# Kernel tuning notes

Hardware: AMD Instinct MI355X
Metric: run time of the kernel (lower is better)

The kernel has to match this reference:

```python
import jax, jax.numpy as jnp
import numpy as np

NPOINT, NSAMPLE, RADIUS = 1024, 32, 0.2
BN_EPS = 1e-5


def _fps(xyz, npoint):
    # Farthest point sampling. Torch version starts from a random index; we use
    # index 0 deterministically (same algorithm, fixed seed point).
    B, N, _ = xyz.shape

    def step(carry, _):
        distance, farthest = carry                               # [B,N], [B]
        centroid = jnp.take_along_axis(xyz, farthest[:, None, None], axis=1)  # [B,1,3]
        d = jnp.sum((xyz - centroid) ** 2, axis=-1)              # [B,N]
        distance = jnp.minimum(distance, d)
        nxt = jnp.argmax(distance, axis=-1).astype(jnp.int32)
        return (distance, nxt), farthest

    init = (jnp.full((B, N), 1e10, xyz.dtype), jnp.zeros((B,), jnp.int32))
    _, cents = jax.lax.scan(step, init, None, length=npoint)     # [npoint,B]
    return jnp.transpose(cents)                                  # [B,npoint]


def _ball_query(radius, nsample, xyz, new_xyz):
    # Sort-based ball query, exactly as the torch reference (pad with first idx).
    B, N, _ = xyz.shape
    sq = -2.0 * jnp.einsum('bsc,bnc->bsn', new_xyz, xyz)
    sq = sq + jnp.sum(new_xyz ** 2, -1)[:, :, None] + jnp.sum(xyz ** 2, -1)[:, None, :]
    idx = jnp.where(sq > radius * radius, N, jnp.arange(N, dtype=jnp.int32))  # [B,S,N]
    idx = jnp.sort(idx, axis=-1)[:, :, :nsample]                 # [B,S,nsample]
    first = idx[:, :, :1]
    return jnp.where(idx == N, first, idx)


def setup_inputs() -> dict:
    key = jax.random.key(0)
    ks = jax.random.split(key, 4)
    B, N = 8, 8192
    d = {"x": jax.random.uniform(ks[0], (B, N, 3), jnp.float32)}
    mlp = [3, 64, 64, 128]
    for i in range(3):
        cin, cout = mlp[i], mlp[i + 1]
        d[f"W{i+1}"] = jax.random.normal(ks[i + 1], (cout, cin), jnp.float32) * 0.1
        d[f"b{i+1}"] = jnp.zeros((cout,), jnp.float32)
        d[f"g{i+1}"] = jnp.ones((cout,), jnp.float32)
        d[f"be{i+1}"] = jnp.zeros((cout,), jnp.float32)
    return d


def reference(x, W1, b1, g1, be1, W2, b2, g2, be2, W3, b3, g3, be3):
    # sample_and_group (points=None)
    cents = _fps(x, NPOINT)                                      # [B,npoint]
    new_x = jnp.take_along_axis(x, cents[:, :, None], axis=1)    # [B,npoint,3]
    idx = _ball_query(RADIUS, NSAMPLE, x, new_x)                 # [B,npoint,nsample]
    grouped = jax.vmap(lambda p, i: p[i])(x, idx)                # [B,npoint,nsample,3]
    h = jnp.transpose(grouped - new_x[:, :, None, :], (0, 3, 2, 1))  # [B,3,nsample,npoint]

    # grouped 1x1 conv + BatchNorm (training-mode batch stats) + ReLU
    for W, b, g, be in ((W1, b1, g1, be1), (W2, b2, g2, be2), (W3, b3, g3, be3)):
        y = jnp.einsum('bcns,oc->bons', h, W) + b[None, :, None, None]
        mean = jnp.mean(y, axis=(0, 2, 3), keepdims=True)
        var = jnp.mean((y - mean) ** 2, axis=(0, 2, 3), keepdims=True)
        h = jax.nn.relu(g[None, :, None, None] * (y - mean) * jax.lax.rsqrt(var + BN_EPS)
                        + be[None, :, None, None])

    out = jnp.transpose(jnp.max(h, axis=2), (0, 2, 1))           # [B,npoint,128]
    return new_x, out
```

## Files before the change

kernel.cpp:

```cpp
#include <hip/hip_runtime.h>
#include <stdint.h>

constexpr int NB = 8;
constexpr int NN = 8192;
constexpr int NS = 1024;
constexpr int NK = 32;
constexpr int PTOT = NB * NS * NK;

#define R2C 0.039999999105930328f

__device__ unsigned short g_cents[NB * NS];
__device__ unsigned short g_idx[NB * NS * NK];
__device__ float g_stat1[12];
__device__ float g_stat2[4160];
__device__ float g_stat3[4160];
__device__ float g_st1[128];
__device__ float g_st2[128];
__device__ float g_st3[256];

__global__ __launch_bounds__(256, 4) void k_zero(){
  const int tid = threadIdx.x;
  for (int i = tid; i < 4160; i += 256){ g_stat2[i] = 0.f; g_stat3[i] = 0.f; }
  if (tid < 12) g_stat1[tid] = 0.f;
}

template<int C, int R>
__device__ __forceinline__ void rstep64(uint32_t& kh, uint32_t& kl){
  uint32_t oh = (uint32_t)__builtin_amdgcn_update_dpp(0, (int)kh, C, R, 0xf, false);
  uint32_t ol = (uint32_t)__builtin_amdgcn_update_dpp(0, (int)kl, C, R, 0xf, false);
  uint64_t o = ((uint64_t)oh << 32) | ol;
  uint64_t k = ((uint64_t)kh << 32) | kl;
  if (o > k){ kh = oh; kl = ol; }
}

__global__ __launch_bounds__(512)
__attribute__((amdgpu_waves_per_eu(2, 2)))
void k_fps(const float* __restrict__ x){
  __shared__ float lp[NN * 3];
  __shared__ uint2 part[16];
  const int b = blockIdx.x;
  const int t = threadIdx.x;
  const int lane = t & 63;
  const int w = t >> 6;
  const float* xb = x + b * NN * 3;
  float px[16], py[16], pz[16], dd[16];
#pragma unroll
  for (int j = 0; j < 16; j++){
    int p = t + 512 * j;
    px[j] = xb[p*3+0]; py[j] = xb[p*3+1]; pz[j] = xb[p*3+2];
    dd[j] = 1e10f;
  }
#pragma unroll
  for (int j = 0; j < 16; j++){
    asm volatile("" : "+v"(px[j]), "+v"(py[j]), "+v"(pz[j]));
  }
  for (int i = t; i < NN*3; i += 512) lp[i] = xb[i];
  float cx = xb[0], cy = xb[1], cz = xb[2];
  if (t == 0) g_cents[b*NS] = 0;
  __syncthreads();
  for (int s = 0; s < NS-1; s++){
    float bv = -1.0f; int bi = 0x7fffffff;
#pragma unroll
    for (int j = 0; j < 16; j++){
      float dx = __fsub_rn(px[j], cx);
      float dy = __fsub_rn(py[j], cy);
      float dz = __fsub_rn(pz[j], cz);
      float d  = __fadd_rn(__fadd_rn(__fmul_rn(dx,dx), __fmul_rn(dy,dy)), __fmul_rn(dz,dz));
      float nd = fminf(dd[j], d);
      dd[j] = nd;
      if (nd > bv){ bv = nd; bi = t + 512*j; }
    }
    uint32_t kh = __float_as_uint(bv);
    uint32_t kl = ~(uint32_t)bi;
    rstep64<0x111, 0xf>(kh, kl);
    rstep64<0x112, 0xf>(kh, kl);
    rstep64<0x114, 0xf>(kh, kl);
    rstep64<0x118, 0xf>(kh, kl);
    rstep64<0x142, 0xa>(kh, kl);
    rstep64<0x143, 0xc>(kh, kl);
    const int pb = (s & 1) << 3;
    if (lane == 63) part[pb + w] = make_uint2(kl, kh);
    asm volatile("s_waitcnt lgkmcnt(0)\n\ts_barrier" ::: "memory");
    uint2 pr = part[pb + (lane & 7)];
    uint32_t qh = pr.y, ql = pr.x;
    rstep64<0x111, 0xf>(qh, ql);
    rstep64<0x112, 0xf>(qh, ql);
    rstep64<0x114, 0xf>(qh, ql);
    int widx = ~__builtin_amdgcn_readlane((int)ql, 7);
    const float* cp = lp + widx*3;
    cx = cp[0]; cy = cp[1]; cz = cp[2];
    if (t == 0) g_cents[b*NS + s + 1] = (unsigned short)widx;
  }
}

__device__ __forceinline__ void ballq_wave(const float* __restrict__ xb,
                                           int c, unsigned short* og,
                                           float* __restrict__ oc){
  const int lane = threadIdx.x & 63;
  const float ax = xb[c*3+0], ay = xb[c*3+1], az = xb[c*3+2];
  if (lane == 0){ oc[0] = ax; oc[1] = ay; oc[2] = az; }
  const float na = __fadd_rn(__fadd_rn(__fmul_rn(ax,ax), __fmul_rn(ay,ay)), __fmul_rn(az,az));
  int cnt = 0, first = -1;
  for (int base = 0; base < NN && cnt < NK; base += 64){
    int n = base + lane;
    float bx = xb[n*3+0], by = xb[n*3+1], bz = xb[n*3+2];
    float dot = __fadd_rn(__fadd_rn(__fmul_rn(ax,bx), __fmul_rn(ay,by)), __fmul_rn(az,bz));
    float nb  = __fadd_rn(__fadd_rn(__fmul_rn(bx,bx), __fmul_rn(by,by)), __fmul_rn(bz,bz));
    float sq  = __fadd_rn(__fadd_rn(__fmul_rn(-2.0f, dot), na), nb);
    bool valid = !(sq > R2C);
    unsigned long long m = __ballot(valid);
    if (first < 0 && m) first = base + (int)__builtin_ctzll(m);
    int pre = __popcll(m & ((1ull << lane) - 1ull));
    int pos = cnt + pre;
    if (valid && pos < NK) og[pos] = (unsigned short)n;
    cnt += __popcll(m);
  }
  if (cnt < NK && lane >= cnt && lane < NK) og[lane] = (unsigned short)first;
}

__global__ __launch_bounds__(256, 4) void k_ballq(const float* __restrict__ x,
                                                  float* __restrict__ out){
  const int g = blockIdx.x * 4 + (threadIdx.x >> 6);
  const float* xb = x + (g >> 10) * NN * 3;
  ballq_wave(xb, (int)g_cents[g], g_idx + (size_t)g * NK, out + (size_t)g * 3);
}

__global__ __launch_bounds__(256, 4) void k_stat1(const float* __restrict__ x){
  __shared__ unsigned int idxs_u[512];
  __shared__ float gc[32][3];
  unsigned short* idxs = (unsigned short*)idxs_u;
  const int tid = threadIdx.x;
  const int g0 = blockIdx.x * 32;
  const float* xb = x + (g0 >> 10) * NN * 3;
  for (int i = tid; i < 512; i += 256)
    idxs_u[i] = ((const unsigned int*)(g_idx + (size_t)g0 * NK))[i];
  if (tid < 32){
    int cc = g_cents[g0 + tid];
    gc[tid][0]=xb[cc*3+0]; gc[tid][1]=xb[cc*3+1]; gc[tid][2]=xb[cc*3+2];
  }
  __syncthreads();
  float a[12];
#pragma unroll
  for (int i = 0; i < 12; i++) a[i] = 0.f;
  for (int u = 0; u < 4; u++){
    int sid = u*256 + tid;
    int lg = sid >> 5, kk = sid & 31;
    int ii = idxs[lg*32 + kk];
    float hx = xb[ii*3+0] - gc[lg][0];
    float hy = xb[ii*3+1] - gc[lg][1];
    float hz = xb[ii*3+2] - gc[lg][2];
    a[0]+=hx; a[1]+=hy; a[2]+=hz;
    a[3]+=hx*hx; a[4]+=hx*hy; a[5]+=hx*hz;
    a[6]+=hy*hx; a[7]+=hy*hy; a[8]+=hy*hz;
    a[9]+=hz*hx; a[10]+=hz*hy; a[11]+=hz*hz;
  }
#pragma unroll
  for (int i = 0; i < 12; i++){
#pragma unroll
    for (int off = 32; off > 0; off >>= 1) a[i] += __shfl_down(a[i], off);
  }
  if ((tid & 63) == 0){
#pragma unroll
    for (int i = 0; i < 12; i++) atomicAdd(&g_stat1[i], a[i]);
  }
}

__global__ __launch_bounds__(256, 4) void k_fold(const float* __restrict__ W,
                       const float* __restrict__ gg,
                       const float* __restrict__ be,
                       int which, int Cin, int Cout){
  const float* stats = (which == 0) ? g_stat1 : (which == 1) ? g_stat2 : g_stat3;
  float* st = (which == 0) ? g_st1 : (which == 1) ? g_st2 : g_st3;
  __shared__ float mu[64];
  __shared__ float part[256];
  const int tid = threadIdx.x;
  const int nparts = 256 / Cout;
  const int c = tid % Cout;
  const int prt = tid / Cout;
  const float invP = 1.0f / (float)PTOT;
  if (tid < Cin) mu[tid] = stats[tid] * invP;
  __syncthreads();
  float q = 0.f;
  for (int i = prt; i < Cin; i += nparts){
    float wi = W[c*Cin + i];
    float r = 0.f;
    for (int j = 0; j < Cin; j++)
      r += stats[Cin + i*Cin + j] * invP * W[c*Cin + j];
    q += wi * r;
  }
  part[tid] = q;
  __syncthreads();
  if (prt == 0){
    for (int p2 = 1; p2 < nparts; p2++) q += part[p2*Cout + c];
    float ml = 0.f;
    for (int j = 0; j < Cin; j++) ml += W[c*Cin + j] * mu[j];
    float var = q - ml*ml;
    float inv = 1.0f / sqrtf(var + 1e-5f);
    float sc = gg[c] * inv;
    float tc = be[c] - sc * ml;
    st[c] = sc; st[Cout + c] = tc;
  }
}

__global__ __launch_bounds__(256, 2) void k_stat2(const float* __restrict__ x,
                                                  const float* __restrict__ W1){
  __shared__ unsigned int idxs_u[512];
  __shared__ float gc[32][3];
  __shared__ float w1t[3][64];
  __shared__ float s1v[64], t1v[64];
  __shared__ float tile[128*68];
  __shared__ float muacc[64];
  unsigned short* idxs = (unsigned short*)idxs_u;
  const int tid = threadIdx.x;
  const int g0 = blockIdx.x * 32;
  const float* xb = x + (g0 >> 10) * NN * 3;
  for (int i = tid; i < 512; i += 256)
    idxs_u[i] = ((const unsigned int*)(g_idx + (size_t)g0 * NK))[i];
  if (tid < 32){
    int cc = g_cents[g0 + tid];
    gc[tid][0]=xb[cc*3+0]; gc[tid][1]=xb[cc*3+1]; gc[tid][2]=xb[cc*3+2];
  }
  if (tid < 64){
    w1t[0][tid]=W1[tid*3+0]; w1t[1][tid]=W1[tid*3+1]; w1t[2][tid]=W1[tid*3+2];
    s1v[tid]=g_st1[tid]; t1v[tid]=g_st1[64+tid];
    muacc[tid]=0.f;
  }
  float acc[4][4];
#pragma unroll
  for (int r=0;r<4;r++)
#pragma unroll
    for (int q=0;q<4;q++) acc[r][q]=0.f;
  const int ti = tid & 15, tj = tid >> 4;
  const int pl = tid & 127;
  const int ch0 = (tid >> 7) * 32;
  __syncthreads();
  for (int u = 0; u < 8; u++){
    int sid = u*128 + pl;
    int lg = sid >> 5, kk = sid & 31;
    int ii = idxs[lg*32 + kk];
    float hx = xb[ii*3+0] - gc[lg][0];
    float hy = xb[ii*3+1] - gc[lg][1];
    float hz = xb[ii*3+2] - gc[lg][2];
    float* row = &tile[pl*68 + ch0];
#pragma unroll
    for (int cq = 0; cq < 8; cq++){
      int c = ch0 + cq*4;
      float y0 = fmaf(w1t[0][c+0],hx, fmaf(w1t[1][c+0],hy, w1t[2][c+0]*hz));
      float y1 = fmaf(w1t[0][c+1],hx, fmaf(w1t[1][c+1],hy, w1t[2][c+1]*hz));
      float y2 = fmaf(w1t[0][c+2],hx, fmaf(w1t[1][c+2],hy, w1t[2][c+2]*hz));
      float y3 = fmaf(w1t[0][c+3],hx, fmaf(w1t[1][c+3],hy, w1t[2][c+3]*hz));
      float4 hv;
      hv.x = fmaxf(fmaf(s1v[c+0],y0,t1v[c+0]), 0.f);
      hv.y = fmaxf(fmaf(s1v[c+1],y1,t1v[c+1]), 0.f);
      hv.z = fmaxf(fmaf(s1v[c+2],y2,t1v[c+2]), 0.f);
      hv.w = fmaxf(fmaf(s1v[c+3],y3,t1v[c+3]), 0.f);
      *(float4*)&row[cq*4] = hv;
    }
    __syncthreads();
    const float4* t4 = (const float4*)tile;
#pragma unroll 4
    for (int p = 0; p < 128; p++){
      float4 av = t4[p*17 + ti];
      float4 bv = t4[p*17 + tj];
      acc[0][0]=fmaf(av.x,bv.x,acc[0][0]); acc[0][1]=fmaf(av.x,bv.y,acc[0][1]);
      acc[0][2]=fmaf(av.x,bv.z,acc[0][2]); acc[0][3]=fmaf(av.x,bv.w,acc[0][3]);
      acc[1][0]=fmaf(av.y,bv.x,acc[1][0]); acc[1][1]=fmaf(av.y,bv.y,acc[1][1]);
      acc[1][2]=fmaf(av.y,bv.z,acc[1][2]); acc[1][3]=fmaf(av.y,bv.w,acc[1][3]);
      acc[2][0]=fmaf(av.z,bv.x,acc[2][0]); acc[2][1]=fmaf(av.z,bv.y,acc[2][1]);
      acc[2][2]=fmaf(av.z,bv.z,acc[2][2]); acc[2][3]=fmaf(av.z,bv.w,acc[2][3]);
      acc[3][0]=fmaf(av.w,bv.x,acc[3][0]); acc[3][1]=fmaf(av.w,bv.y,acc[3][1]);
      acc[3][2]=fmaf(av.w,bv.z,acc[3][2]); acc[3][3]=fmaf(av.w,bv.w,acc[3][3]);
    }
    if (tid < 64){
      float m = 0.f;
      for (int p = 0; p < 128; p++) m += tile[p*68 + tid];
      muacc[tid] += m;
    }
    __syncthreads();
  }
  if (tid < 64) atomicAdd(&g_stat2[tid], muacc[tid]);
#pragma unroll
  for (int r=0;r<4;r++)
#pragma unroll
    for (int q=0;q<4;q++)
      atomicAdd(&g_stat2[64 + (ti*4+r)*64 + (tj*4+q)], acc[r][q]);
}

__global__ __launch_bounds__(256, 2) void k_stat3(const float* __restrict__ x,
                                                  const float* __restrict__ W1,
                                                  const float* __restrict__ W2){
  __shared__ unsigned int idxs_u[512];
  __shared__ float gc[32][3];
  __shared__ float w1t[3][64];
  __shared__ float s1v[64], t1v[64], s2v[64], t2v[64];
  __shared__ float w2f[4096];
  __shared__ float tile[128*68];
  __shared__ float muacc[64];
  unsigned short* idxs = (unsigned short*)idxs_u;
  const int tid = threadIdx.x;
  const int g0 = blockIdx.x * 32;
  const float* xb = x + (g0 >> 10) * NN * 3;
  for (int i = tid; i < 512; i += 256)
    idxs_u[i] = ((const unsigned int*)(g_idx + (size_t)g0 * NK))[i];
  if (tid < 32){
    int cc = g_cents[g0 + tid];
    gc[tid][0]=xb[cc*3+0]; gc[tid][1]=xb[cc*3+1]; gc[tid][2]=xb[cc*3+2];
  }
  if (tid < 64){
    w1t[0][tid]=W1[tid*3+0]; w1t[1][tid]=W1[tid*3+1]; w1t[2][tid]=W1[tid*3+2];
    s1v[tid]=g_st1[tid]; t1v[tid]=g_st1[64+tid];
    s2v[tid]=g_st2[tid]; t2v[tid]=g_st2[64+tid];
    muacc[tid]=0.f;
  }
#pragma unroll
  for (int e = 0; e < 16; e++) w2f[tid + e*256] = W2[tid + e*256];
  float acc[4][4];
#pragma unroll
  for (int r=0;r<4;r++)
#pragma unroll
    for (int q=0;q<4;q++) acc[r][q]=0.f;
  const int ti = tid & 15, tj = tid >> 4;
  const int pl = tid & 127;
  const int ch0 = (tid >> 7) * 32;
  __syncthreads();
  for (int u = 0; u < 8; u++){
    int sid = u*128 + pl;
    int lg = sid >> 5, kk = sid & 31;
    int ii = idxs[lg*32 + kk];
    float hx = xb[ii*3+0] - gc[lg][0];
    float hy = xb[ii*3+1] - gc[lg][1];
    float hz = xb[ii*3+2] - gc[lg][2];
    float h2r[64];
#pragma unroll
    for (int c = 0; c < 64; c++){
      float y = fmaf(w1t[0][c],hx, fmaf(w1t[1][c],hy, w1t[2][c]*hz));
      h2r[c] = fmaxf(fmaf(s1v[c],y,t1v[c]), 0.f);
    }
    float* row = &tile[pl*68];
    for (int c = ch0; c < ch0 + 32; c++){
      const float4* wr = (const float4*)&w2f[c*64];
      float y = 0.f;
#pragma unroll
      for (int j4 = 0; j4 < 16; j4++){
        float4 wv = wr[j4];
        y = fmaf(wv.x, h2r[j4*4+0], y);
        y = fmaf(wv.y, h2r[j4*4+1], y);
        y = fmaf(wv.z, h2r[j4*4+2], y);
        y = fmaf(wv.w, h2r[j4*4+3], y);
      }
      row[c] = fmaxf(fmaf(s2v[c], y, t2v[c]), 0.f);
    }
    __syncthreads();
    const float4* t4 = (const float4*)tile;
#pragma unroll 4
    for (int p = 0; p < 128; p++){
      float4 av = t4[p*17 + ti];
      float4 bv = t4[p*17 + tj];
      acc[0][0]=fmaf(av.x,bv.x,acc[0][0]); acc[0][1]=fmaf(av.x,bv.y,acc[0][1]);
      acc[0][2]=fmaf(av.x,bv.z,acc[0][2]); acc[0][3]=fmaf(av.x,bv.w,acc[0][3]);
      acc[1][0]=fmaf(av.y,bv.x,acc[1][0]); acc[1][1]=fmaf(av.y,bv.y,acc[1][1]);
      acc[1][2]=fmaf(av.y,bv.z,acc[1][2]); acc[1][3]=fmaf(av.y,bv.w,acc[1][3]);
      acc[2][0]=fmaf(av.z,bv.x,acc[2][0]); acc[2][1]=fmaf(av.z,bv.y,acc[2][1]);
      acc[2][2]=fmaf(av.z,bv.z,acc[2][2]); acc[2][3]=fmaf(av.z,bv.w,acc[2][3]);
      acc[3][0]=fmaf(av.w,bv.x,acc[3][0]); acc[3][1]=fmaf(av.w,bv.y,acc[3][1]);
      acc[3][2]=fmaf(av.w,bv.z,acc[3][2]); acc[3][3]=fmaf(av.w,bv.w,acc[3][3]);
    }
    if (tid < 64){
      float m = 0.f;
      for (int p = 0; p < 128; p++) m += tile[p*68 + tid];
      muacc[tid] += m;
    }
    __syncthreads();
  }
  if (tid < 64) atomicAdd(&g_stat3[tid], muacc[tid]);
#pragma unroll
  for (int r=0;r<4;r++)
#pragma unroll
    for (int q=0;q<4;q++)
      atomicAdd(&g_stat3[64 + (ti*4+r)*64 + (tj*4+q)], acc[r][q]);
}

__global__ __launch_bounds__(256, 2) void k_final(const float* __restrict__ x,
    const float* __restrict__ W1,
    const float* __restrict__ W2,
    const float* __restrict__ W3,
    float* __restrict__ out){
  __shared__ unsigned int idxs_u[64];
  __shared__ float gc[4][3];
  __shared__ float w1t[3][64];
  __shared__ float s1v[64], t1v[64], s2v[64], t2v[64], s3v[128], t3v[128];
  __shared__ float h2t[32*68];
  __shared__ float h3t[32*68];
  __shared__ float mx[2][128];
  unsigned short* idxs = (unsigned short*)idxs_u;
  const int tid = threadIdx.x;
  const int g0 = blockIdx.x * 4;
  const float* xb = x + (g0 >> 10) * NN * 3;
  if (tid < 64) idxs_u[tid] = ((const unsigned int*)(g_idx + (size_t)g0 * NK))[tid];
  if (tid < 4){
    int cc = g_cents[g0 + tid];
    gc[tid][0]=xb[cc*3+0]; gc[tid][1]=xb[cc*3+1]; gc[tid][2]=xb[cc*3+2];
  }
  if (tid < 64){
    w1t[0][tid]=W1[tid*3+0]; w1t[1][tid]=W1[tid*3+1]; w1t[2][tid]=W1[tid*3+2];
    s1v[tid]=g_st1[tid]; t1v[tid]=g_st1[64+tid];
    s2v[tid]=g_st2[tid]; t2v[tid]=g_st2[64+tid];
  }
  if (tid < 128){ s3v[tid]=g_st3[tid]; t3v[tid]=g_st3[128+tid]; }
  __syncthreads();
  for (int gi = 0; gi < 4; gi++){
#pragma unroll
    for (int u = 0; u < 8; u++){
      int v = tid + u * 256;
      int kk = v >> 6, c = v & 63;
      int ii = idxs[gi*32 + kk];
      float hx = xb[ii*3+0] - gc[gi][0];
      float hy = xb[ii*3+1] - gc[gi][1];
      float hz = xb[ii*3+2] - gc[gi][2];
      float y = fmaf(w1t[0][c],hx, fmaf(w1t[1][c],hy, w1t[2][c]*hz));
      h2t[kk*68 + c] = fmaxf(fmaf(s1v[c], y, t1v[c]), 0.f);
    }
    __syncthreads();
    {
      const int c2 = tid & 63, kq = tid >> 6;
      float wv2[64];
      const float4* wrow = (const float4*)(W2 + c2*64);
#pragma unroll
      for (int q = 0; q < 16; q++){
        float4 uv = wrow[q];
        wv2[q*4+0]=uv.x; wv2[q*4+1]=uv.y; wv2[q*4+2]=uv.z; wv2[q*4+3]=uv.w;
      }
#pragma unroll
      for (int k2 = 0; k2 < 8; k2++){
        int kk = kq*8 + k2;
        const float4* hr = (const float4*)&h2t[kk*68];
        float y = 0.f;
#pragma unroll
        for (int j4 = 0; j4 < 16; j4++){
          float4 hv = hr[j4];
          y = fmaf(wv2[j4*4+0], hv.x, y);
          y = fmaf(wv2[j4*4+1], hv.y, y);
          y = fmaf(wv2[j4*4+2], hv.z, y);
          y = fmaf(wv2[j4*4+3], hv.w, y);
        }
        h3t[kk*68 + c2] = fmaxf(fmaf(s2v[c2], y, t2v[c2]), 0.f);
      }
    }
    __syncthreads();
    {
      const int c3 = tid & 127, half = tid >> 7;
      float wv3[64];
      const float4* wrow = (const float4*)(W3 + c3*64);
#pragma unroll
      for (int q = 0; q < 16; q++){
        float4 uv = wrow[q];
        wv3[q*4+0]=uv.x; wv3[q*4+1]=uv.y; wv3[q*4+2]=uv.z; wv3[q*4+3]=uv.w;
      }
      float m = -1e30f;
#pragma unroll
      for (int k2 = 0; k2 < 16; k2++){
        int kk = half*16 + k2;
        const float4* hr = (const float4*)&h3t[kk*68];
        float y = 0.f;
#pragma unroll
        for (int j4 = 0; j4 < 16; j4++){
          float4 hv = hr[j4];
          y = fmaf(wv3[j4*4+0], hv.x, y);
          y = fmaf(wv3[j4*4+1], hv.y, y);
          y = fmaf(wv3[j4*4+2], hv.z, y);
          y = fmaf(wv3[j4*4+3], hv.w, y);
        }
        float h4 = fmaxf(fmaf(s3v[c3], y, t3v[c3]), 0.f);
        m = fmaxf(m, h4);
      }
      mx[half][c3] = m;
    }
    __syncthreads();
    if (tid < 128){
      float m = fmaxf(mx[0][tid], mx[1][tid]);
      out[24576 + ((g0 + gi) << 7) + tid] = m;
    }
    __syncthreads();
  }
}

extern "C" void kernel_launch(void* const* d_in, const int* in_sizes, int n_in,
                              void* d_out, int out_size, void* d_ws, size_t ws_size,
                              hipStream_t stream){
  const float* x   = (const float*)d_in[0];
  const float* W1  = (const float*)d_in[1];
  const float* g1  = (const float*)d_in[3];
  const float* be1 = (const float*)d_in[4];
  const float* W2  = (const float*)d_in[5];
  const float* g2  = (const float*)d_in[7];
  const float* be2 = (const float*)d_in[8];
  const float* W3  = (const float*)d_in[9];
  const float* g3  = (const float*)d_in[11];
  const float* be3 = (const float*)d_in[12];
  float* out = (float*)d_out;
  (void)d_ws; (void)ws_size; (void)in_sizes; (void)n_in; (void)out_size;

  k_zero<<<1, 256, 0, stream>>>();
  k_fps<<<NB, 512, 0, stream>>>(x);
  k_ballq<<<(NB*NS)/4, 256, 0, stream>>>(x, out);
  k_stat1<<<256, 256, 0, stream>>>(x);
  k_fold<<<1, 256, 0, stream>>>(W1, g1, be1, 0, 3, 64);
  k_stat2<<<256, 256, 0, stream>>>(x, W1);
  k_fold<<<1, 256, 0, stream>>>(W2, g2, be2, 1, 64, 64);
  k_stat3<<<256, 256, 0, stream>>>(x, W1, W2);
  k_fold<<<1, 256, 0, stream>>>(W3, g3, be3, 2, 64, 128);
  k_final<<<2048, 256, 0, stream>>>(x, W1, W2, W3, out);
}
```

Measured before the change: 2.063 ms.

## Vectorize FPS distance loop with packed float2 and stage BN fold in LDS

The FPS inner loop now works on two points per operation using float2 vectors, so the compiler can emit packed FP32 math. The running argmax is split across four independent accumulators to shorten the dependency chain, and the new centroid's coordinates are prefetched from float4 LDS in parallel with the cross-wave reduction, then broadcast via readlane. The fold kernel copies W and the covariance stats into padded shared memory instead of rereading global memory in its inner loop. Risks are different rounding, since contraction is disabled, and a subtle tie-break ordering change.

```diff
diff --git a/kernel.cpp b/kernel.cpp
--- a/kernel.cpp
+++ b/kernel.cpp
@@ -8,6 +8,8 @@
 constexpr int PTOT = NB * NS * NK;
 
 #define R2C 0.039999999105930328f
+
+typedef float v2f __attribute__((ext_vector_type(2)));
 
 __device__ unsigned short g_cents[NB * NS];
 __device__ unsigned short g_idx[NB * NS * NK];
@@ -36,41 +38,67 @@
 __global__ __launch_bounds__(512)
 __attribute__((amdgpu_waves_per_eu(2, 2)))
 void k_fps(const float* __restrict__ x){
-  __shared__ float lp[NN * 3];
+#pragma clang fp contract(off)
+  __shared__ float4 lp4[NN];
   __shared__ uint2 part[16];
   const int b = blockIdx.x;
   const int t = threadIdx.x;
   const int lane = t & 63;
   const int w = t >> 6;
   const float* xb = x + b * NN * 3;
-  float px[16], py[16], pz[16], dd[16];
-#pragma unroll
-  for (int j = 0; j < 16; j++){
-    int p = t + 512 * j;
-    px[j] = xb[p*3+0]; py[j] = xb[p*3+1]; pz[j] = xb[p*3+2];
-    dd[j] = 1e10f;
-  }
-#pragma unroll
-  for (int j = 0; j < 16; j++){
-    asm volatile("" : "+v"(px[j]), "+v"(py[j]), "+v"(pz[j]));
-  }
-  for (int i = t; i < NN*3; i += 512) lp[i] = xb[i];
+  v2f px2[8], py2[8], pz2[8], dd2[8];
+#pragma unroll
+  for (int j = 0; j < 8; j++){
+    int p0 = t + 1024 * j;
+    int p1 = p0 + 512;
+    px2[j] = (v2f){xb[p0*3+0], xb[p1*3+0]};
+    py2[j] = (v2f){xb[p0*3+1], xb[p1*3+1]};
+    pz2[j] = (v2f){xb[p0*3+2], xb[p1*3+2]};
+    dd2[j] = (v2f){1e10f, 1e10f};
+  }
+#pragma unroll
+  for (int j = 0; j < 8; j++){
+    asm volatile("" : "+v"(px2[j]), "+v"(py2[j]), "+v"(pz2[j]));
+  }
+  for (int i = t; i < NN; i += 512){
+    lp4[i] = make_float4(xb[i*3+0], xb[i*3+1], xb[i*3+2], 0.f);
+  }
   float cx = xb[0], cy = xb[1], cz = xb[2];
   if (t == 0) g_cents[b*NS] = 0;
   __syncthreads();
   for (int s = 0; s < NS-1; s++){
-    float bv = -1.0f; int bi = 0x7fffffff;
-#pragma unroll
-    for (int j = 0; j < 16; j++){
-      float dx = __fsub_rn(px[j], cx);
-      float dy = __fsub_rn(py[j], cy);
-      float dz = __fsub_rn(pz[j], cz);
-      float d  = __fadd_rn(__fadd_rn(__fmul_rn(dx,dx), __fmul_rn(dy,dy)), __fmul_rn(dz,dz));
-      float nd = fminf(dd[j], d);
-      dd[j] = nd;
-      if (nd > bv){ bv = nd; bi = t + 512*j; }
-    }
-    uint32_t kh = __float_as_uint(bv);
+    float bvA = -1.0f, bvB = -1.0f, bvC = -1.0f, bvD = -1.0f;
+    int   jbA = 16,    jbB = 16,    jbC = 16,    jbD = 16;
+#pragma unroll
+    for (int j = 0; j < 8; j++){
+      v2f dx = px2[j] - cx;
+      v2f dy = py2[j] - cy;
+      v2f dz = pz2[j] - cz;
+      v2f sx = dx * dx;
+      v2f sy = dy * dy;
+      v2f sz = dz * dz;
+      v2f d  = (sx + sy) + sz;
+      float n0 = fminf(dd2[j].x, d.x);
+      float n1 = fminf(dd2[j].y, d.y);
+      dd2[j].x = n0; dd2[j].y = n1;
+      if ((j & 1) == 0){
+        if (n0 > bvA){ bvA = n0; jbA = 2*j; }
+        if (n1 > bvB){ bvB = n1; jbB = 2*j + 1; }
+      } else {
+        if (n0 > bvC){ bvC = n0; jbC = 2*j; }
+        if (n1 > bvD){ bvD = n1; jbD = 2*j + 1; }
+      }
+    }
+    {
+      bool tk1 = (bvB > bvA) || ((bvB == bvA) && (jbB < jbA));
+      float m1v = tk1 ? bvB : bvA; int m1j = tk1 ? jbB : jbA;
+      bool tk2 = (bvD > bvC) || ((bvD == bvC) && (jbD < jbC));
+      float m2v = tk2 ? bvD : bvC; int m2j = tk2 ? jbD : jbC;
+      bool tk3 = (m2v > m1v) || ((m2v == m1v) && (m2j < m1j));
+      bvA = tk3 ? m2v : m1v; jbA = tk3 ? m2j : m1j;
+    }
+    const int bi = t + (jbA << 9);
+    uint32_t kh = __float_as_uint(bvA);
     uint32_t kl = ~(uint32_t)bi;
     rstep64<0x111, 0xf>(kh, kl);
     rstep64<0x112, 0xf>(kh, kl);
@@ -82,13 +110,18 @@
     if (lane == 63) part[pb + w] = make_uint2(kl, kh);
     asm volatile("s_waitcnt lgkmcnt(0)\n\ts_barrier" ::: "memory");
     uint2 pr = part[pb + (lane & 7)];
+    int cidx = ~(int)pr.x;
+    float4 cc = lp4[cidx];
     uint32_t qh = pr.y, ql = pr.x;
     rstep64<0x111, 0xf>(qh, ql);
     rstep64<0x112, 0xf>(qh, ql);
     rstep64<0x114, 0xf>(qh, ql);
     int widx = ~__builtin_amdgcn_readlane((int)ql, 7);
-    const float* cp = lp + widx*3;
-    cx = cp[0]; cy = cp[1]; cz = cp[2];
+    unsigned long long mk = __ballot(cidx == widx);
+    int src = (int)__builtin_ctzll(mk);
+    cx = __int_as_float(__builtin_amdgcn_readlane(__float_as_int(cc.x), src));
+    cy = __int_as_float(__builtin_amdgcn_readlane(__float_as_int(cc.y), src));
+    cz = __int_as_float(__builtin_amdgcn_readlane(__float_as_int(cc.z), src));
     if (t == 0) g_cents[b*NS + s + 1] = (unsigned short)widx;
   }
 }
@@ -172,28 +205,32 @@
   const float* stats = (which == 0) ? g_stat1 : (which == 1) ? g_stat2 : g_stat3;
   float* st = (which == 0) ? g_st1 : (which == 1) ? g_st2 : g_st3;
   __shared__ float mu[64];
-  __shared__ float part[256];
+  __shared__ float partl[256];
+  __shared__ float s_l[64*65];
+  __shared__ float w_l[128*65];
   const int tid = threadIdx.x;
+  const float invP = 1.0f / (float)PTOT;
+  for (int i = tid; i < Cout*Cin; i += 256) w_l[(i/Cin)*65 + (i%Cin)] = W[i];
+  for (int i = tid; i < Cin*Cin; i += 256) s_l[(i/Cin)*65 + (i%Cin)] = stats[Cin + i] * invP;
+  if (tid < Cin) mu[tid] = stats[tid] * invP;
+  __syncthreads();
   const int nparts = 256 / Cout;
   const int c = tid % Cout;
   const int prt = tid / Cout;
-  const float invP = 1.0f / (float)PTOT;
-  if (tid < Cin) mu[tid] = stats[tid] * invP;
-  __syncthreads();
   float q = 0.f;
   for (int i = prt; i < Cin; i += nparts){
-    float wi = W[c*Cin + i];
+    float wi = w_l[c*65 + i];
     float r = 0.f;
     for (int j = 0; j < Cin; j++)
-      r += stats[Cin + i*Cin + j] * invP * W[c*Cin + j];
+      r += s_l[i*65 + j] * w_l[c*65 + j];
     q += wi * r;
   }
-  part[tid] = q;
+  partl[tid] = q;
   __syncthreads();
   if (prt == 0){
-    for (int p2 = 1; p2 < nparts; p2++) q += part[p2*Cout + c];
+    for (int p2 = 1; p2 < nparts; p2++) q += partl[p2*Cout + c];
     float ml = 0.f;
-    for (int j = 0; j < Cin; j++) ml += W[c*Cin + j] * mu[j];
+    for (int j = 0; j < Cin; j++) ml += w_l[c*65 + j] * mu[j];
     float var = q - ml*ml;
     float inv = 1.0f / sqrtf(var + 1e-5f);
     float sc = gg[c] * inv;
```

New measurement: 1.910 ms. 7.4% less time.
